# Optimization experiments

Measured on AMD Instinct MI355X. Metric: run time of the kernel, lower is better.

The kernel has to match this reference:

```python
import jax, jax.numpy as jnp
import numpy as np
from math import factorial, sqrt

# Irreps config (all even parity): (mul, l)
IRREPS_IN1 = [(128, 0), (64, 1), (32, 2)]   # dim 480
IRREPS_IN2 = [(1, 0), (1, 1), (1, 2)]       # dim 9
OUT_LS = (0, 1, 2)
Z = 50000


def _su2_cg(j1, j2, j3, m1, m2, m3):
    """Complex SU(2) Clebsch-Gordan coefficient <j1 m1 j2 m2 | j3 m3> (integer l)."""
    if m3 != m1 + m2:
        return 0.0
    pref = sqrt((2 * j3 + 1) * factorial(j3 + j1 - j2) * factorial(j3 - j1 + j2)
                * factorial(j1 + j2 - j3) / factorial(j1 + j2 + j3 + 1))
    pref *= sqrt(factorial(j3 + m3) * factorial(j3 - m3) * factorial(j1 - m1)
                 * factorial(j1 + m1) * factorial(j2 - m2) * factorial(j2 + m2))
    s = 0.0
    for k in range(max(0, j2 - j3 - m1, j1 - j3 + m2),
                   min(j1 + j2 - j3, j1 - m1, j2 + m2) + 1):
        s += (-1) ** k / (factorial(k) * factorial(j1 + j2 - j3 - k)
                          * factorial(j1 - m1 - k) * factorial(j2 + m2 - k)
                          * factorial(j3 - j2 + m1 + k) * factorial(j3 - j1 - m2 + k))
    return pref * s


def _q_real_to_complex(l):
    """e3nn change-of-basis real->complex spherical harmonics."""
    q = np.zeros((2 * l + 1, 2 * l + 1), dtype=np.complex128)
    for m in range(-l, 0):
        q[l + m, l + abs(m)] = 1 / np.sqrt(2)
        q[l + m, l - abs(m)] = -1j / np.sqrt(2)
    q[l, l] = 1.0
    for m in range(1, l + 1):
        q[l + m, l + abs(m)] = (-1) ** m / np.sqrt(2)
        q[l + m, l - abs(m)] = 1j * (-1) ** m / np.sqrt(2)
    return (-1j) ** l * q


def _w3j(l1, l2, l3):
    """Real-basis Wigner 3j tensor, unit Frobenius norm (e3nn convention)."""
    C = np.zeros((2 * l1 + 1, 2 * l2 + 1, 2 * l3 + 1))
    for m1 in range(-l1, l1 + 1):
        for m2 in range(-l2, l2 + 1):
            m3 = m1 + m2
            if -l3 <= m3 <= l3:
                C[l1 + m1, l2 + m2, l3 + m3] = _su2_cg(l1, l2, l3, m1, m2, m3)
    Q1, Q2, Q3 = _q_real_to_complex(l1), _q_real_to_complex(l2), _q_real_to_complex(l3)
    Cr = np.einsum('ij,kl,nm,ikn->jlm', Q1, Q2, np.conj(Q3), C.astype(np.complex128))
    assert np.abs(Cr.imag).max() < 1e-8
    Cr = Cr.real
    return (Cr / np.linalg.norm(Cr)).astype(np.float32)


def _build_instructions():
    off1 = np.cumsum([0] + [m * (2 * l + 1) for m, l in IRREPS_IN1])
    off2 = np.cumsum([0] + [m * (2 * l + 1) for m, l in IRREPS_IN2])
    instrs = []
    for i, (mul1, l1) in enumerate(IRREPS_IN1):
        for j, (mul2, l2) in enumerate(IRREPS_IN2):
            for l3 in range(abs(l1 - l2), l1 + l2 + 1):
                if l3 in OUT_LS or l3 == 0:
                    # path_weight: irrep_normalization='component', path_normalization='element';
                    # each i_out is unique so fan-in = mul2 (uvu num_elements)
                    instrs.append(dict(s1=int(off1[i]), mul1=mul1, l1=l1,
                                       s2=int(off2[j]), mul2=mul2, l2=l2,
                                       l3=l3, pw=sqrt((2 * l3 + 1) / mul2)))
    return instrs


INSTRS = _build_instructions()
DIM1 = sum(m * (2 * l + 1) for m, l in IRREPS_IN1)                 # 480
DIM2 = sum(m * (2 * l + 1) for m, l in IRREPS_IN2)                 # 9
WEIGHT_NUMEL = sum(i['mul1'] * i['mul2'] for i in INSTRS)          # 960
DIM_OUT = sum(i['mul1'] * (2 * i['l3'] + 1) for i in INSTRS)       # 3136
W3J = {(l1, l2, l3): jnp.asarray(_w3j(l1, l2, l3))
       for (l1, l2, l3) in {(i['l1'], i['l2'], i['l3']) for i in INSTRS}}


def setup_inputs() -> dict:
    key = jax.random.key(0)
    k1, k2, k3 = jax.random.split(key, 3)
    x = jax.random.normal(k1, (Z, DIM1), dtype=jnp.float32)
    y = jax.random.normal(k2, (Z, DIM2), dtype=jnp.float32)
    weight = jax.random.normal(k3, (Z, WEIGHT_NUMEL), dtype=jnp.float32)
    return {"x": x, "y": y, "weight": weight}


def reference(x, y, weight):
    z = x.shape[0]
    outs = []
    wo = 0
    for ins in INSTRS:
        mul1, l1, mul2, l2, l3 = ins['mul1'], ins['l1'], ins['mul2'], ins['l2'], ins['l3']
        d1, d2, d3 = 2 * l1 + 1, 2 * l2 + 1, 2 * l3 + 1
        x_s = x[:, ins['s1']:ins['s1'] + mul1 * d1].reshape(z, mul1, d1)
        y_s = y[:, ins['s2']:ins['s2'] + mul2 * d2].reshape(z, mul2, d2)
        w_s = weight[:, wo:wo + mul1 * mul2].reshape(z, mul1, mul2)
        wo += mul1 * mul2
        C = W3J[(l1, l2, l3)]  # [d1, d2, d3]
        # uvu: out[z,u,k] = pw * sum_{v,i,j} w[z,u,v] * C[i,j,k] * x[z,u,i] * y[z,v,j]
        o = ins['pw'] * jnp.einsum('ijk,zui,zvj,zuv->zuk', C, x_s, y_s, w_s)
        outs.append(o.reshape(z, mul1 * d3))
    return jnp.concatenate(outs, axis=-1)  # [Z, 3136]
```

## Files before the change

### kernel.cpp

```cpp
#include <hip/hip_runtime.h>
#include <cmath>
#include <complex>


struct W3JPack {
    float c000[1];
    float c011[9];
    float c022[25];
    float c101[9];
    float c110[9];
    float c111[27];
    float c112[45];
    float c121[45];
    float c122[75];
    float c202[25];
    float c211[45];
    float c212[75];
    float c220[25];
    float c221[75];
    float c222[125];
};

namespace {

using cd = std::complex<double>;

double factd(int n) { double r = 1.0; for (int i = 2; i <= n; ++i) r *= i; return r; }

double su2_cg(int j1, int j2, int j3, int m1, int m2, int m3) {
    if (m3 != m1 + m2) return 0.0;
    double pref = std::sqrt((2.0 * j3 + 1.0) * factd(j3 + j1 - j2) * factd(j3 - j1 + j2)
                            * factd(j1 + j2 - j3) / factd(j1 + j2 + j3 + 1));
    pref *= std::sqrt(factd(j3 + m3) * factd(j3 - m3) * factd(j1 - m1)
                      * factd(j1 + m1) * factd(j2 - m2) * factd(j2 + m2));
    int kmin = 0;
    if (j2 - j3 - m1 > kmin) kmin = j2 - j3 - m1;
    if (j1 - j3 + m2 > kmin) kmin = j1 - j3 + m2;
    int kmax = j1 + j2 - j3;
    if (j1 - m1 < kmax) kmax = j1 - m1;
    if (j2 + m2 < kmax) kmax = j2 + m2;
    double s = 0.0;
    for (int k = kmin; k <= kmax; ++k) {
        double den = factd(k) * factd(j1 + j2 - j3 - k) * factd(j1 - m1 - k)
                   * factd(j2 + m2 - k) * factd(j3 - j2 + m1 + k) * factd(j3 - j1 - m2 + k);
        s += ((k & 1) ? -1.0 : 1.0) / den;
    }
    return pref * s;
}

void qmat(int l, cd q[5][5]) {
    for (int a = 0; a < 5; ++a) for (int b = 0; b < 5; ++b) q[a][b] = cd(0, 0);
    const double is2 = 1.0 / std::sqrt(2.0);
    for (int m = -l; m < 0; ++m) {
        q[l + m][l - m] = cd(is2, 0.0);
        q[l + m][l + m] = cd(0.0, -is2);
    }
    q[l][l] = cd(1.0, 0.0);
    for (int m = 1; m <= l; ++m) {
        double sgn = (m & 1) ? -1.0 : 1.0;
        q[l + m][l + m] = cd(sgn * is2, 0.0);
        q[l + m][l - m] = cd(0.0, sgn * is2);
    }
    cd f(1.0, 0.0);
    const cd mi(0.0, -1.0);
    for (int k = 0; k < l; ++k) f *= mi;
    for (int a = 0; a < 5; ++a) for (int b = 0; b < 5; ++b) q[a][b] *= f;
}

void w3j_real(int l1, int l2, int l3, float* out, double pw) {
    const int d1 = 2 * l1 + 1, d2 = 2 * l2 + 1, d3 = 2 * l3 + 1;
    cd Q1[5][5], Q2[5][5], Q3[5][5];
    qmat(l1, Q1); qmat(l2, Q2); qmat(l3, Q3);
    double tmp[125];
    double norm2 = 0.0;
    for (int a = 0; a < d1; ++a)
        for (int b = 0; b < d2; ++b)
            for (int c = 0; c < d3; ++c) {
                cd acc(0.0, 0.0);
                for (int i = 0; i < d1; ++i) {
                    int m1 = i - l1;
                    for (int k = 0; k < d2; ++k) {
                        int m2 = k - l2;
                        int m3 = m1 + m2;
                        if (m3 < -l3 || m3 > l3) continue;
                        double cg = su2_cg(l1, l2, l3, m1, m2, m3);
                        if (cg == 0.0) continue;
                        acc += Q1[i][a] * Q2[k][b] * std::conj(Q3[m3 + l3][c]) * cg;
                    }
                }
                double v = acc.real();
                tmp[(a * d2 + b) * d3 + c] = v;
                norm2 += v * v;
            }
    const double scale = pw / std::sqrt(norm2);
    for (int idx = 0; idx < d1 * d2 * d3; ++idx) out[idx] = (float)(tmp[idx] * scale);
}

W3JPack build_pack() {
    W3JPack p;
    const double s3 = std::sqrt(3.0), s5 = std::sqrt(5.0);
    w3j_real(0, 0, 0, p.c000, 1.0);
    w3j_real(0, 1, 1, p.c011, s3);
    w3j_real(0, 2, 2, p.c022, s5);
    w3j_real(1, 0, 1, p.c101, s3);
    w3j_real(1, 1, 0, p.c110, 1.0);
    w3j_real(1, 1, 1, p.c111, s3);
    w3j_real(1, 1, 2, p.c112, s5);
    w3j_real(1, 2, 1, p.c121, s3);
    w3j_real(1, 2, 2, p.c122, s5);
    w3j_real(2, 0, 2, p.c202, s5);
    w3j_real(2, 1, 1, p.c211, s3);
    w3j_real(2, 1, 2, p.c212, s5);
    w3j_real(2, 2, 0, p.c220, 1.0);
    w3j_real(2, 2, 1, p.c221, s3);
    w3j_real(2, 2, 2, p.c222, s5);
    return p;
}

const W3JPack g_pack = build_pack();

}


__global__ __launch_bounds__(256) void dtp_kernel(
    const float* __restrict__ x, const float* __restrict__ y,
    const float* __restrict__ w, float* __restrict__ out,
    const W3JPack P, int Z)
{
    const int t = blockIdx.x * 256 + threadIdx.x;
    const int N0 = Z * 128;
    const int N1 = Z * 64;

    if (t < N0) {
        const int z = t >> 7, u = t & 127;
        const float* xz = x + (size_t)z * 480;
        const float* yz = y + (size_t)z * 9;
        const float* wz = w + (size_t)z * 960;
        float* oz = out + (size_t)z * 3136;

        const float xv = xz[u];
        const float y0 = yz[0];
        float y1[3], y2[5];
#pragma unroll
        for (int j = 0; j < 3; ++j) y1[j] = yz[1 + j];
#pragma unroll
        for (int j = 0; j < 5; ++j) y2[j] = yz[4 + j];

        oz[u] = wz[u] * (P.c000[0] * xv * y0);
        {
            const float wx = wz[128 + u] * xv;
#pragma unroll
            for (int k = 0; k < 3; ++k) {
                float s = 0.f;
#pragma unroll
                for (int j = 0; j < 3; ++j) s += P.c011[j * 3 + k] * y1[j];
                oz[128 + 3 * u + k] = wx * s;
            }
        }
        {
            const float wx = wz[256 + u] * xv;
#pragma unroll
            for (int k = 0; k < 5; ++k) {
                float s = 0.f;
#pragma unroll
                for (int j = 0; j < 5; ++j) s += P.c022[j * 5 + k] * y2[j];
                oz[512 + 5 * u + k] = wx * s;
            }
        }
    } else if (t < N0 + N1) {
        const int tt = t - N0;
        const int z = tt >> 6, u = tt & 63;
        const float* xz = x + (size_t)z * 480 + 128 + 3 * u;
        const float* yz = y + (size_t)z * 9;
        const float* wz = w + (size_t)z * 960;
        float* oz = out + (size_t)z * 3136;

        float xv[3];
#pragma unroll
        for (int i = 0; i < 3; ++i) xv[i] = xz[i];
        const float y0 = yz[0];
        float y1[3], y2[5];
#pragma unroll
        for (int j = 0; j < 3; ++j) y1[j] = yz[1 + j];
#pragma unroll
        for (int j = 0; j < 5; ++j) y2[j] = yz[4 + j];

        float xy1[3][3], xy2[3][5];
#pragma unroll
        for (int i = 0; i < 3; ++i) {
#pragma unroll
            for (int j = 0; j < 3; ++j) xy1[i][j] = xv[i] * y1[j];
#pragma unroll
            for (int j = 0; j < 5; ++j) xy2[i][j] = xv[i] * y2[j];
        }

        {
            const float wy = wz[384 + u] * y0;
#pragma unroll
            for (int k = 0; k < 3; ++k) {
                float s = 0.f;
#pragma unroll
                for (int i = 0; i < 3; ++i) s += P.c101[i * 3 + k] * xv[i];
                oz[1152 + 3 * u + k] = wy * s;
            }
        }
        {
            float s = 0.f;
#pragma unroll
            for (int i = 0; i < 3; ++i)
#pragma unroll
                for (int j = 0; j < 3; ++j) s += P.c110[i * 3 + j] * xy1[i][j];
            oz[1344 + u] = wz[448 + u] * s;
        }
        {
            const float wv = wz[512 + u];
#pragma unroll
            for (int k = 0; k < 3; ++k) {
                float s = 0.f;
#pragma unroll
                for (int i = 0; i < 3; ++i)
#pragma unroll
                    for (int j = 0; j < 3; ++j) s += P.c111[(i * 3 + j) * 3 + k] * xy1[i][j];
                oz[1408 + 3 * u + k] = wv * s;
            }
        }
        {
            const float wv = wz[576 + u];
#pragma unroll
            for (int k = 0; k < 5; ++k) {
                float s = 0.f;
#pragma unroll
                for (int i = 0; i < 3; ++i)
#pragma unroll
                    for (int j = 0; j < 3; ++j) s += P.c112[(i * 3 + j) * 5 + k] * xy1[i][j];
                oz[1600 + 5 * u + k] = wv * s;
            }
        }
        {
            const float wv = wz[640 + u];
#pragma unroll
            for (int k = 0; k < 3; ++k) {
                float s = 0.f;
#pragma unroll
                for (int i = 0; i < 3; ++i)
#pragma unroll
                    for (int j = 0; j < 5; ++j) s += P.c121[(i * 5 + j) * 3 + k] * xy2[i][j];
                oz[1920 + 3 * u + k] = wv * s;
            }
        }
        {
            const float wv = wz[704 + u];
#pragma unroll
            for (int k = 0; k < 5; ++k) {
                float s = 0.f;
#pragma unroll
                for (int i = 0; i < 3; ++i)
#pragma unroll
                    for (int j = 0; j < 5; ++j) s += P.c122[(i * 5 + j) * 5 + k] * xy2[i][j];
                oz[2112 + 5 * u + k] = wv * s;
            }
        }
    } else {
        const int tt = t - N0 - N1;
        if (tt >= Z * 32) return;
        const int z = tt >> 5, u = tt & 31;
        const float* xz = x + (size_t)z * 480 + 320 + 5 * u;
        const float* yz = y + (size_t)z * 9;
        const float* wz = w + (size_t)z * 960;
        float* oz = out + (size_t)z * 3136;

        float xv[5];
#pragma unroll
        for (int i = 0; i < 5; ++i) xv[i] = xz[i];
        const float y0 = yz[0];
        float y1[3], y2[5];
#pragma unroll
        for (int j = 0; j < 3; ++j) y1[j] = yz[1 + j];
#pragma unroll
        for (int j = 0; j < 5; ++j) y2[j] = yz[4 + j];

        float xy1[5][3], xy2[5][5];
#pragma unroll
        for (int i = 0; i < 5; ++i) {
#pragma unroll
            for (int j = 0; j < 3; ++j) xy1[i][j] = xv[i] * y1[j];
#pragma unroll
            for (int j = 0; j < 5; ++j) xy2[i][j] = xv[i] * y2[j];
        }

        {
            const float wy = wz[768 + u] * y0;
#pragma unroll
            for (int k = 0; k < 5; ++k) {
                float s = 0.f;
#pragma unroll
                for (int i = 0; i < 5; ++i) s += P.c202[i * 5 + k] * xv[i];
                oz[2432 + 5 * u + k] = wy * s;
            }
        }
        {
            const float wv = wz[800 + u];
#pragma unroll
            for (int k = 0; k < 3; ++k) {
                float s = 0.f;
#pragma unroll
                for (int i = 0; i < 5; ++i)
#pragma unroll
                    for (int j = 0; j < 3; ++j) s += P.c211[(i * 3 + j) * 3 + k] * xy1[i][j];
                oz[2592 + 3 * u + k] = wv * s;
            }
        }
        {
            const float wv = wz[832 + u];
#pragma unroll
            for (int k = 0; k < 5; ++k) {
                float s = 0.f;
#pragma unroll
                for (int i = 0; i < 5; ++i)
#pragma unroll
                    for (int j = 0; j < 3; ++j) s += P.c212[(i * 3 + j) * 5 + k] * xy1[i][j];
                oz[2688 + 5 * u + k] = wv * s;
            }
        }
        {
            float s = 0.f;
#pragma unroll
            for (int i = 0; i < 5; ++i)
#pragma unroll
                for (int j = 0; j < 5; ++j) s += P.c220[i * 5 + j] * xy2[i][j];
            oz[2848 + u] = wz[864 + u] * s;
        }
        {
            const float wv = wz[896 + u];
#pragma unroll
            for (int k = 0; k < 3; ++k) {
                float s = 0.f;
#pragma unroll
                for (int i = 0; i < 5; ++i)
#pragma unroll
                    for (int j = 0; j < 5; ++j) s += P.c221[(i * 5 + j) * 3 + k] * xy2[i][j];
                oz[2880 + 3 * u + k] = wv * s;
            }
        }
        {
            const float wv = wz[928 + u];
#pragma unroll
            for (int k = 0; k < 5; ++k) {
                float s = 0.f;
#pragma unroll
                for (int i = 0; i < 5; ++i)
#pragma unroll
                    for (int j = 0; j < 5; ++j) s += P.c222[(i * 5 + j) * 5 + k] * xy2[i][j];
                oz[2976 + 5 * u + k] = wv * s;
            }
        }
    }
}

extern "C" void kernel_launch(void* const* d_in, const int* in_sizes, int n_in,
                              void* d_out, int out_size, void* d_ws, size_t ws_size,
                              hipStream_t stream)
{
    const float* x = (const float*)d_in[0];
    const float* y = (const float*)d_in[1];
    const float* w = (const float*)d_in[2];
    float* out = (float*)d_out;

    const int Z = in_sizes[0] / 480;
    const int total = Z * 224;
    const int grid = (total + 255) / 256;

    hipLaunchKernelGGL(dtp_kernel, dim3(grid), dim3(256), 0, stream,
                       x, y, w, out, g_pack, Z);
}
```

Baseline: 191.7 us.

## Coalesce strided loads and stores via per-wave LDS transpose buffers

Per-thread strided accesses of 3 or 5 consecutive floats, in both the x loads and the multi-component output stores, are replaced by a per-wavefront shared-memory exchange. Each wave writes its values contiguously into LDS and then issues unit-stride global accesses, so every global instruction touches one contiguous span. This targets uncoalesced memory traffic in a bandwidth-bound kernel. The cost is extra LDS traffic, wave barriers and some bank conflicts, and the code relies on each wave mapping to a single z row, which holds given the 64/128/32 thread layout.

```diff
diff --git a/kernel.cpp b/kernel.cpp
--- a/kernel.cpp
+++ b/kernel.cpp
@@ -119,6 +119,61 @@
 
 const W3JPack g_pack = build_pack();
 
+
+}
+
+template<int K>
+__device__ __forceinline__ void xchg_store(float* __restrict__ base,
+                                           const float (&v)[K],
+                                           float* __restrict__ buf, int ln)
+{
+#pragma unroll
+    for (int k = 0; k < K; ++k) buf[K * ln + k] = v[k];
+    __builtin_amdgcn_wave_barrier();
+#pragma unroll
+    for (int s = 0; s < K; ++s) base[64 * s + ln] = buf[64 * s + ln];
+    __builtin_amdgcn_wave_barrier();
+}
+
+template<int K>
+__device__ __forceinline__ void xchg_load(const float* __restrict__ base,
+                                          float (&v)[K],
+                                          float* __restrict__ buf, int ln)
+{
+#pragma unroll
+    for (int s = 0; s < K; ++s) buf[64 * s + ln] = base[64 * s + ln];
+    __builtin_amdgcn_wave_barrier();
+#pragma unroll
+    for (int k = 0; k < K; ++k) v[k] = buf[K * ln + k];
+    __builtin_amdgcn_wave_barrier();
+}
+
+template<int K>
+__device__ __forceinline__ void half_store(float* __restrict__ base_half,
+                                           const float (&v)[K],
+                                           float* __restrict__ buf, int li, int half)
+{
+    float* b = buf + half * K * 32;
+#pragma unroll
+    for (int k = 0; k < K; ++k) b[K * li + k] = v[k];
+    __builtin_amdgcn_wave_barrier();
+#pragma unroll
+    for (int s = 0; s < K; ++s) base_half[32 * s + li] = b[32 * s + li];
+    __builtin_amdgcn_wave_barrier();
+}
+
+template<int K>
+__device__ __forceinline__ void half_load(const float* __restrict__ base_half,
+                                          float (&v)[K],
+                                          float* __restrict__ buf, int li, int half)
+{
+    float* b = buf + half * K * 32;
+#pragma unroll
+    for (int s = 0; s < K; ++s) b[32 * s + li] = base_half[32 * s + li];
+    __builtin_amdgcn_wave_barrier();
+#pragma unroll
+    for (int k = 0; k < K; ++k) v[k] = b[K * li + k];
+    __builtin_amdgcn_wave_barrier();
 }
 
 
@@ -127,12 +182,17 @@
     const float* __restrict__ w, float* __restrict__ out,
     const W3JPack P, int Z)
 {
+    __shared__ float xch[4][320];
+    const int ln = threadIdx.x & 63;
+    float* buf = xch[threadIdx.x >> 6];
+
     const int t = blockIdx.x * 256 + threadIdx.x;
     const int N0 = Z * 128;
     const int N1 = Z * 64;
 
     if (t < N0) {
         const int z = t >> 7, u = t & 127;
+        const int u0 = u & ~63;
         const float* xz = x + (size_t)z * 480;
         const float* yz = y + (size_t)z * 9;
         const float* wz = w + (size_t)z * 960;
@@ -147,37 +207,42 @@
         for (int j = 0; j < 5; ++j) y2[j] = yz[4 + j];
 
         oz[u] = wz[u] * (P.c000[0] * xv * y0);
+
         {
             const float wx = wz[128 + u] * xv;
+            float o[3];
 #pragma unroll
             for (int k = 0; k < 3; ++k) {
                 float s = 0.f;
 #pragma unroll
                 for (int j = 0; j < 3; ++j) s += P.c011[j * 3 + k] * y1[j];
-                oz[128 + 3 * u + k] = wx * s;
-            }
+                o[k] = wx * s;
+            }
+            xchg_store<3>(oz + 128 + 3 * u0, o, buf, ln);
         }
         {
             const float wx = wz[256 + u] * xv;
+            float o[5];
 #pragma unroll
             for (int k = 0; k < 5; ++k) {
                 float s = 0.f;
 #pragma unroll
                 for (int j = 0; j < 5; ++j) s += P.c022[j * 5 + k] * y2[j];
-                oz[512 + 5 * u + k] = wx * s;
-            }
+                o[k] = wx * s;
+            }
+            xchg_store<5>(oz + 512 + 5 * u0, o, buf, ln);
         }
     } else if (t < N0 + N1) {
         const int tt = t - N0;
-        const int z = tt >> 6, u = tt & 63;
-        const float* xz = x + (size_t)z * 480 + 128 + 3 * u;
+        const int z = tt >> 6;
+        const int u = ln;
         const float* yz = y + (size_t)z * 9;
         const float* wz = w + (size_t)z * 960;
         float* oz = out + (size_t)z * 3136;
 
         float xv[3];
-#pragma unroll
-        for (int i = 0; i < 3; ++i) xv[i] = xz[i];
+        xchg_load<3>(x + (size_t)z * 480 + 128, xv, buf, ln);
+
         const float y0 = yz[0];
         float y1[3], y2[5];
 #pragma unroll
@@ -196,13 +261,15 @@
 
         {
             const float wy = wz[384 + u] * y0;
+            float o[3];
 #pragma unroll
             for (int k = 0; k < 3; ++k) {
                 float s = 0.f;
 #pragma unroll
                 for (int i = 0; i < 3; ++i) s += P.c101[i * 3 + k] * xv[i];
-                oz[1152 + 3 * u + k] = wy * s;
-            }
+                o[k] = wy * s;
+            }
+            xchg_store<3>(oz + 1152, o, buf, ln);
         }
         {
             float s = 0.f;
@@ -214,6 +281,7 @@
         }
         {
             const float wv = wz[512 + u];
+            float o[3];
 #pragma unroll
             for (int k = 0; k < 3; ++k) {
                 float s = 0.f;
@@ -221,11 +289,13 @@
                 for (int i = 0; i < 3; ++i)
 #pragma unroll
                     for (int j = 0; j < 3; ++j) s += P.c111[(i * 3 + j) * 3 + k] * xy1[i][j];
-                oz[1408 + 3 * u + k] = wv * s;
-            }
+                o[k] = wv * s;
+            }
+            xchg_store<3>(oz + 1408, o, buf, ln);
         }
         {
             const float wv = wz[576 + u];
+            float o[5];
 #pragma unroll
             for (int k = 0; k < 5; ++k) {
                 float s = 0.f;
@@ -233,11 +303,13 @@
                 for (int i = 0; i < 3; ++i)
 #pragma unroll
                     for (int j = 0; j < 3; ++j) s += P.c112[(i * 3 + j) * 5 + k] * xy1[i][j];
-                oz[1600 + 5 * u + k] = wv * s;
-            }
+                o[k] = wv * s;
+            }
+            xchg_store<5>(oz + 1600, o, buf, ln);
         }
         {
             const float wv = wz[640 + u];
+            float o[3];
 #pragma unroll
             for (int k = 0; k < 3; ++k) {
                 float s = 0.f;
@@ -245,11 +317,13 @@
                 for (int i = 0; i < 3; ++i)
 #pragma unroll
                     for (int j = 0; j < 5; ++j) s += P.c121[(i * 5 + j) * 3 + k] * xy2[i][j];
-                oz[1920 + 3 * u + k] = wv * s;
-            }
+                o[k] = wv * s;
+            }
+            xchg_store<3>(oz + 1920, o, buf, ln);
         }
         {
             const float wv = wz[704 + u];
+            float o[5];
 #pragma unroll
             for (int k = 0; k < 5; ++k) {
                 float s = 0.f;
@@ -257,21 +331,23 @@
                 for (int i = 0; i < 3; ++i)
 #pragma unroll
                     for (int j = 0; j < 5; ++j) s += P.c122[(i * 5 + j) * 5 + k] * xy2[i][j];
-                oz[2112 + 5 * u + k] = wv * s;
-            }
+                o[k] = wv * s;
+            }
+            xchg_store<5>(oz + 2112, o, buf, ln);
         }
     } else {
         const int tt = t - N0 - N1;
         if (tt >= Z * 32) return;
-        const int z = tt >> 5, u = tt & 31;
-        const float* xz = x + (size_t)z * 480 + 320 + 5 * u;
+        const int z = tt >> 5;
+        const int u = tt & 31;
+        const int li = ln & 31, half = ln >> 5;
         const float* yz = y + (size_t)z * 9;
         const float* wz = w + (size_t)z * 960;
         float* oz = out + (size_t)z * 3136;
 
         float xv[5];
-#pragma unroll
-        for (int i = 0; i < 5; ++i) xv[i] = xz[i];
+        half_load<5>(x + (size_t)z * 480 + 320, xv, buf, li, half);
+
         const float y0 = yz[0];
         float y1[3], y2[5];
 #pragma unroll
@@ -290,16 +366,19 @@
 
         {
             const float wy = wz[768 + u] * y0;
+            float o[5];
 #pragma unroll
             for (int k = 0; k < 5; ++k) {
                 float s = 0.f;
 #pragma unroll
                 for (int i = 0; i < 5; ++i) s += P.c202[i * 5 + k] * xv[i];
-                oz[2432 + 5 * u + k] = wy * s;
-            }
+                o[k] = wy * s;
+            }
+            half_store<5>(oz + 2432, o, buf, li, half);
         }
         {
             const float wv = wz[800 + u];
+            float o[3];
 #pragma unroll
             for (int k = 0; k < 3; ++k) {
                 float s = 0.f;
@@ -307,11 +386,13 @@
                 for (int i = 0; i < 5; ++i)
 #pragma unroll
                     for (int j = 0; j < 3; ++j) s += P.c211[(i * 3 + j) * 3 + k] * xy1[i][j];
-                oz[2592 + 3 * u + k] = wv * s;
-            }
+                o[k] = wv * s;
+            }
+            half_store<3>(oz + 2592, o, buf, li, half);
         }
         {
             const float wv = wz[832 + u];
+            float o[5];
 #pragma unroll
             for (int k = 0; k < 5; ++k) {
                 float s = 0.f;
@@ -319,8 +400,9 @@
                 for (int i = 0; i < 5; ++i)
 #pragma unroll
                     for (int j = 0; j < 3; ++j) s += P.c212[(i * 3 + j) * 5 + k] * xy1[i][j];
-                oz[2688 + 5 * u + k] = wv * s;
-            }
+                o[k] = wv * s;
+            }
+            half_store<5>(oz + 2688, o, buf, li, half);
         }
         {
             float s = 0.f;
@@ -332,6 +414,7 @@
         }
         {
             const float wv = wz[896 + u];
+            float o[3];
 #pragma unroll
             for (int k = 0; k < 3; ++k) {
                 float s = 0.f;
@@ -339,11 +422,13 @@
                 for (int i = 0; i < 5; ++i)
 #pragma unroll
                     for (int j = 0; j < 5; ++j) s += P.c221[(i * 5 + j) * 3 + k] * xy2[i][j];
-                oz[2880 + 3 * u + k] = wv * s;
-            }
+                o[k] = wv * s;
+            }
+            half_store<3>(oz + 2880, o, buf, li, half);
         }
         {
             const float wv = wz[928 + u];
+            float o[5];
 #pragma unroll
             for (int k = 0; k < 5; ++k) {
                 float s = 0.f;
@@ -351,8 +436,9 @@
                 for (int i = 0; i < 5; ++i)
 #pragma unroll
                     for (int j = 0; j < 5; ++j) s += P.c222[(i * 5 + j) * 5 + k] * xy2[i][j];
-                oz[2976 + 5 * u + k] = wv * s;
-            }
+                o[k] = wv * s;
+            }
+            half_store<5>(oz + 2976, o, buf, li, half);
         }
     }
 }
```

Measured after the change: 186.6 us. 2.7% less time.

## Stage outputs in per-wave LDS and write with coalesced float4 stores; interleave block types

Applied to the files above, without the earlier changes.

Each wave now writes its results into a per-wave shared-memory buffer and then stores them to global memory as contiguous float4 vectors, replacing the strided per-lane scalar stores. The x inputs for l=1 and l=2 are loaded the same way, vectorised through LDS. A block-index swizzle interleaves l0, l1 and l2 work within groups of seven blocks so the different per-thread costs are spread across the GPU, and the row index is made wave-uniform with readfirstlane. The change adds about 22 KB of LDS per block, which may lower occupancy. It relies on wave-level barriers and on the wave size being 64.

```diff
diff --git a/kernel.cpp b/kernel.cpp
--- a/kernel.cpp
+++ b/kernel.cpp
@@ -125,20 +125,201 @@
 __global__ __launch_bounds__(256) void dtp_kernel(
     const float* __restrict__ x, const float* __restrict__ y,
     const float* __restrict__ w, float* __restrict__ out,
-    const W3JPack P, int Z)
+    const W3JPack P, int Z, int swz)
 {
-    const int t = blockIdx.x * 256 + threadIdx.x;
+    __shared__ __align__(16) float xch[4][1408];
+    const int tid = threadIdx.x;
+    const int ln = tid & 63;
+    float* buf = xch[tid >> 6];
+    float4* bf4 = (float4*)buf;
+
     const int N0 = Z * 128;
     const int N1 = Z * 64;
 
+    int t;
+    if (swz) {
+        const int bid = blockIdx.x;
+        const int q = bid / 7, r = bid - 7 * q;
+        if (r < 4)       t = (4 * q + r) * 256 + tid;
+        else if (r < 6)  t = N0 + (2 * q + (r - 4)) * 256 + tid;
+        else             t = N0 + N1 + q * 256 + tid;
+    } else {
+        t = blockIdx.x * 256 + tid;
+        if (t >= Z * 224) return;
+    }
+
     if (t < N0) {
         const int z = t >> 7, u = t & 127;
-        const float* xz = x + (size_t)z * 480;
+        const int u0 = u & 64;
+        const int zu = __builtin_amdgcn_readfirstlane(z);
+        const float* xz = x + (size_t)zu * 480;
+        const float* yz = y + (size_t)zu * 9;
+        const float* wz = w + (size_t)zu * 960;
+        float* oz = out + (size_t)zu * 3136;
+
+        const float xv = xz[u];
+        const float y0 = yz[0];
+        float y1[3], y2[5];
+#pragma unroll
+        for (int j = 0; j < 3; ++j) y1[j] = yz[1 + j];
+#pragma unroll
+        for (int j = 0; j < 5; ++j) y2[j] = yz[4 + j];
+
+        buf[ln] = wz[u] * (P.c000[0] * xv * y0);
+        {
+            const float wx = wz[128 + u] * xv;
+#pragma unroll
+            for (int k = 0; k < 3; ++k) {
+                float s = 0.f;
+#pragma unroll
+                for (int j = 0; j < 3; ++j) s += P.c011[j * 3 + k] * y1[j];
+                buf[64 + 3 * ln + k] = wx * s;
+            }
+        }
+        {
+            const float wx = wz[256 + u] * xv;
+#pragma unroll
+            for (int k = 0; k < 5; ++k) {
+                float s = 0.f;
+#pragma unroll
+                for (int j = 0; j < 5; ++j) s += P.c022[j * 5 + k] * y2[j];
+                buf[256 + 5 * ln + k] = wx * s;
+            }
+        }
+        __builtin_amdgcn_wave_barrier();
+        if (ln < 16) *(float4*)(oz + u0 + 4 * ln) = bf4[ln];
+        if (ln < 48) *(float4*)(oz + 128 + 3 * u0 + 4 * ln) = bf4[16 + ln];
+        *(float4*)(oz + 512 + 5 * u0 + 4 * ln) = bf4[64 + ln];
+        if (ln < 16) *(float4*)(oz + 512 + 5 * u0 + 256 + 4 * ln) = bf4[128 + ln];
+        __builtin_amdgcn_wave_barrier();
+    } else if (t < N0 + N1) {
+        const int tt = t - N0;
+        const int z = tt >> 6;
+        const int u = ln;
+        const int zu = __builtin_amdgcn_readfirstlane(z);
+        const float* yz = y + (size_t)zu * 9;
+        const float* wz = w + (size_t)zu * 960;
+        float* oz = out + (size_t)zu * 3136;
+
+        {
+            const float4* xs = (const float4*)(x + (size_t)zu * 480 + 128);
+            if (ln < 48) *(float4*)(buf + 4 * ln) = xs[ln];
+        }
+        __builtin_amdgcn_wave_barrier();
+        float xv[3];
+#pragma unroll
+        for (int i = 0; i < 3; ++i) xv[i] = buf[3 * ln + i];
+        __builtin_amdgcn_wave_barrier();
+
+        const float y0 = yz[0];
+        float y1[3], y2[5];
+#pragma unroll
+        for (int j = 0; j < 3; ++j) y1[j] = yz[1 + j];
+#pragma unroll
+        for (int j = 0; j < 5; ++j) y2[j] = yz[4 + j];
+
+        float xy1[3][3], xy2[3][5];
+#pragma unroll
+        for (int i = 0; i < 3; ++i) {
+#pragma unroll
+            for (int j = 0; j < 3; ++j) xy1[i][j] = xv[i] * y1[j];
+#pragma unroll
+            for (int j = 0; j < 5; ++j) xy2[i][j] = xv[i] * y2[j];
+        }
+
+        {
+            const float wy = wz[384 + u] * y0;
+#pragma unroll
+            for (int k = 0; k < 3; ++k) {
+                float s = 0.f;
+#pragma unroll
+                for (int i = 0; i < 3; ++i) s += P.c101[i * 3 + k] * xv[i];
+                buf[3 * ln + k] = wy * s;
+            }
+        }
+        {
+            float s = 0.f;
+#pragma unroll
+            for (int i = 0; i < 3; ++i)
+#pragma unroll
+                for (int j = 0; j < 3; ++j) s += P.c110[i * 3 + j] * xy1[i][j];
+            buf[192 + ln] = wz[448 + u] * s;
+        }
+        {
+            const float wv = wz[512 + u];
+#pragma unroll
+            for (int k = 0; k < 3; ++k) {
+                float s = 0.f;
+#pragma unroll
+                for (int i = 0; i < 3; ++i)
+#pragma unroll
+                    for (int j = 0; j < 3; ++j) s += P.c111[(i * 3 + j) * 3 + k] * xy1[i][j];
+                buf[256 + 3 * ln + k] = wv * s;
+            }
+        }
+        {
+            const float wv = wz[576 + u];
+#pragma unroll
+            for (int k = 0; k < 5; ++k) {
+                float s = 0.f;
+#pragma unroll
+                for (int i = 0; i < 3; ++i)
+#pragma unroll
+                    for (int j = 0; j < 3; ++j) s += P.c112[(i * 3 + j) * 5 + k] * xy1[i][j];
+                buf[448 + 5 * ln + k] = wv * s;
+            }
+        }
+        {
+            const float wv = wz[640 + u];
+#pragma unroll
+            for (int k = 0; k < 3; ++k) {
+                float s = 0.f;
+#pragma unroll
+                for (int i = 0; i < 3; ++i)
+#pragma unroll
+                    for (int j = 0; j < 5; ++j) s += P.c121[(i * 5 + j) * 3 + k] * xy2[i][j];
+                buf[768 + 3 * ln + k] = wv * s;
+            }
+        }
+        {
+            const float wv = wz[704 + u];
+#pragma unroll
+            for (int k = 0; k < 5; ++k) {
+                float s = 0.f;
+#pragma unroll
+                for (int i = 0; i < 3; ++i)
+#pragma unroll
+                    for (int j = 0; j < 5; ++j) s += P.c122[(i * 5 + j) * 5 + k] * xy2[i][j];
+                buf[960 + 5 * ln + k] = wv * s;
+            }
+        }
+        __builtin_amdgcn_wave_barrier();
+        float* ob = oz + 1152;
+#pragma unroll
+        for (int it = 0; it < 5; ++it)
+            *(float4*)(ob + 4 * (it * 64 + ln)) = bf4[it * 64 + ln];
+        __builtin_amdgcn_wave_barrier();
+    } else {
+        const int tt = t - N0 - N1;
+        const int li = ln & 31, half = ln >> 5;
+        const int z0 = __builtin_amdgcn_readfirstlane(tt >> 5);
+        const int z = z0 + half;
+        const int u = li;
         const float* yz = y + (size_t)z * 9;
         const float* wz = w + (size_t)z * 960;
         float* oz = out + (size_t)z * 3136;
 
-        const float xv = xz[u];
+        {
+            const float4* xs = (const float4*)(x + (size_t)z * 480 + 320);
+            *(float4*)(buf + 160 * half + 4 * li) = xs[li];
+            if (li < 8) *(float4*)(buf + 160 * half + 128 + 4 * li) = xs[32 + li];
+        }
+        __builtin_amdgcn_wave_barrier();
+        float xv[5];
+#pragma unroll
+        for (int i = 0; i < 5; ++i) xv[i] = buf[160 * half + 5 * li + i];
+        __builtin_amdgcn_wave_barrier();
+
         const float y0 = yz[0];
         float y1[3], y2[5];
 #pragma unroll
@@ -146,214 +327,89 @@
 #pragma unroll
         for (int j = 0; j < 5; ++j) y2[j] = yz[4 + j];
 
-        oz[u] = wz[u] * (P.c000[0] * xv * y0);
-        {
-            const float wx = wz[128 + u] * xv;
-#pragma unroll
-            for (int k = 0; k < 3; ++k) {
-                float s = 0.f;
-#pragma unroll
-                for (int j = 0; j < 3; ++j) s += P.c011[j * 3 + k] * y1[j];
-                oz[128 + 3 * u + k] = wx * s;
-            }
-        }
-        {
-            const float wx = wz[256 + u] * xv;
-#pragma unroll
-            for (int k = 0; k < 5; ++k) {
-                float s = 0.f;
-#pragma unroll
-                for (int j = 0; j < 5; ++j) s += P.c022[j * 5 + k] * y2[j];
-                oz[512 + 5 * u + k] = wx * s;
-            }
-        }
-    } else if (t < N0 + N1) {
-        const int tt = t - N0;
-        const int z = tt >> 6, u = tt & 63;
-        const float* xz = x + (size_t)z * 480 + 128 + 3 * u;
-        const float* yz = y + (size_t)z * 9;
-        const float* wz = w + (size_t)z * 960;
-        float* oz = out + (size_t)z * 3136;
-
-        float xv[3];
-#pragma unroll
-        for (int i = 0; i < 3; ++i) xv[i] = xz[i];
-        const float y0 = yz[0];
-        float y1[3], y2[5];
-#pragma unroll
-        for (int j = 0; j < 3; ++j) y1[j] = yz[1 + j];
-#pragma unroll
-        for (int j = 0; j < 5; ++j) y2[j] = yz[4 + j];
-
-        float xy1[3][3], xy2[3][5];
-#pragma unroll
-        for (int i = 0; i < 3; ++i) {
+        float xy1[5][3], xy2[5][5];
+#pragma unroll
+        for (int i = 0; i < 5; ++i) {
 #pragma unroll
             for (int j = 0; j < 3; ++j) xy1[i][j] = xv[i] * y1[j];
 #pragma unroll
             for (int j = 0; j < 5; ++j) xy2[i][j] = xv[i] * y2[j];
         }
 
-        {
-            const float wy = wz[384 + u] * y0;
-#pragma unroll
-            for (int k = 0; k < 3; ++k) {
-                float s = 0.f;
-#pragma unroll
-                for (int i = 0; i < 3; ++i) s += P.c101[i * 3 + k] * xv[i];
-                oz[1152 + 3 * u + k] = wy * s;
+        float* hb = buf + 704 * half;
+        {
+            const float wy = wz[768 + u] * y0;
+#pragma unroll
+            for (int k = 0; k < 5; ++k) {
+                float s = 0.f;
+#pragma unroll
+                for (int i = 0; i < 5; ++i) s += P.c202[i * 5 + k] * xv[i];
+                hb[5 * li + k] = wy * s;
+            }
+        }
+        {
+            const float wv = wz[800 + u];
+#pragma unroll
+            for (int k = 0; k < 3; ++k) {
+                float s = 0.f;
+#pragma unroll
+                for (int i = 0; i < 5; ++i)
+#pragma unroll
+                    for (int j = 0; j < 3; ++j) s += P.c211[(i * 3 + j) * 3 + k] * xy1[i][j];
+                hb[160 + 3 * li + k] = wv * s;
+            }
+        }
+        {
+            const float wv = wz[832 + u];
+#pragma unroll
+            for (int k = 0; k < 5; ++k) {
+                float s = 0.f;
+#pragma unroll
+                for (int i = 0; i < 5; ++i)
+#pragma unroll
+                    for (int j = 0; j < 3; ++j) s += P.c212[(i * 3 + j) * 5 + k] * xy1[i][j];
+                hb[256 + 5 * li + k] = wv * s;
             }
         }
         {
             float s = 0.f;
 #pragma unroll
-            for (int i = 0; i < 3; ++i)
-#pragma unroll
-                for (int j = 0; j < 3; ++j) s += P.c110[i * 3 + j] * xy1[i][j];
-            oz[1344 + u] = wz[448 + u] * s;
-        }
-        {
-            const float wv = wz[512 + u];
-#pragma unroll
-            for (int k = 0; k < 3; ++k) {
-                float s = 0.f;
-#pragma unroll
-                for (int i = 0; i < 3; ++i)
-#pragma unroll
-                    for (int j = 0; j < 3; ++j) s += P.c111[(i * 3 + j) * 3 + k] * xy1[i][j];
-                oz[1408 + 3 * u + k] = wv * s;
-            }
-        }
-        {
-            const float wv = wz[576 + u];
-#pragma unroll
-            for (int k = 0; k < 5; ++k) {
-                float s = 0.f;
-#pragma unroll
-                for (int i = 0; i < 3; ++i)
-#pragma unroll
-                    for (int j = 0; j < 3; ++j) s += P.c112[(i * 3 + j) * 5 + k] * xy1[i][j];
-                oz[1600 + 5 * u + k] = wv * s;
-            }
-        }
-        {
-            const float wv = wz[640 + u];
-#pragma unroll
-            for (int k = 0; k < 3; ++k) {
-                float s = 0.f;
-#pragma unroll
-                for (int i = 0; i < 3; ++i)
-#pragma unroll
-                    for (int j = 0; j < 5; ++j) s += P.c121[(i * 5 + j) * 3 + k] * xy2[i][j];
-                oz[1920 + 3 * u + k] = wv * s;
-            }
-        }
-        {
-            const float wv = wz[704 + u];
-#pragma unroll
-            for (int k = 0; k < 5; ++k) {
-                float s = 0.f;
-#pragma unroll
-                for (int i = 0; i < 3; ++i)
-#pragma unroll
-                    for (int j = 0; j < 5; ++j) s += P.c122[(i * 5 + j) * 5 + k] * xy2[i][j];
-                oz[2112 + 5 * u + k] = wv * s;
-            }
-        }
-    } else {
-        const int tt = t - N0 - N1;
-        if (tt >= Z * 32) return;
-        const int z = tt >> 5, u = tt & 31;
-        const float* xz = x + (size_t)z * 480 + 320 + 5 * u;
-        const float* yz = y + (size_t)z * 9;
-        const float* wz = w + (size_t)z * 960;
-        float* oz = out + (size_t)z * 3136;
-
-        float xv[5];
-#pragma unroll
-        for (int i = 0; i < 5; ++i) xv[i] = xz[i];
-        const float y0 = yz[0];
-        float y1[3], y2[5];
-#pragma unroll
-        for (int j = 0; j < 3; ++j) y1[j] = yz[1 + j];
-#pragma unroll
-        for (int j = 0; j < 5; ++j) y2[j] = yz[4 + j];
-
-        float xy1[5][3], xy2[5][5];
-#pragma unroll
-        for (int i = 0; i < 5; ++i) {
-#pragma unroll
-            for (int j = 0; j < 3; ++j) xy1[i][j] = xv[i] * y1[j];
-#pragma unroll
-            for (int j = 0; j < 5; ++j) xy2[i][j] = xv[i] * y2[j];
-        }
-
-        {
-            const float wy = wz[768 + u] * y0;
-#pragma unroll
-            for (int k = 0; k < 5; ++k) {
-                float s = 0.f;
-#pragma unroll
-                for (int i = 0; i < 5; ++i) s += P.c202[i * 5 + k] * xv[i];
-                oz[2432 + 5 * u + k] = wy * s;
-            }
-        }
-        {
-            const float wv = wz[800 + u];
+            for (int i = 0; i < 5; ++i)
+#pragma unroll
+                for (int j = 0; j < 5; ++j) s += P.c220[i * 5 + j] * xy2[i][j];
+            hb[416 + li] = wz[864 + u] * s;
+        }
+        {
+            const float wv = wz[896 + u];
 #pragma unroll
             for (int k = 0; k < 3; ++k) {
                 float s = 0.f;
 #pragma unroll
                 for (int i = 0; i < 5; ++i)
 #pragma unroll
-                    for (int j = 0; j < 3; ++j) s += P.c211[(i * 3 + j) * 3 + k] * xy1[i][j];
-                oz[2592 + 3 * u + k] = wv * s;
-            }
-        }
-        {
-            const float wv = wz[832 + u];
+                    for (int j = 0; j < 5; ++j) s += P.c221[(i * 5 + j) * 3 + k] * xy2[i][j];
+                hb[448 + 3 * li + k] = wv * s;
+            }
+        }
+        {
+            const float wv = wz[928 + u];
 #pragma unroll
             for (int k = 0; k < 5; ++k) {
                 float s = 0.f;
 #pragma unroll
                 for (int i = 0; i < 5; ++i)
 #pragma unroll
-                    for (int j = 0; j < 3; ++j) s += P.c212[(i * 3 + j) * 5 + k] * xy1[i][j];
-                oz[2688 + 5 * u + k] = wv * s;
-            }
-        }
-        {
-            float s = 0.f;
-#pragma unroll
-            for (int i = 0; i < 5; ++i)
-#pragma unroll
-                for (int j = 0; j < 5; ++j) s += P.c220[i * 5 + j] * xy2[i][j];
-            oz[2848 + u] = wz[864 + u] * s;
-        }
-        {
-            const float wv = wz[896 + u];
-#pragma unroll
-            for (int k = 0; k < 3; ++k) {
-                float s = 0.f;
-#pragma unroll
-                for (int i = 0; i < 5; ++i)
-#pragma unroll
-                    for (int j = 0; j < 5; ++j) s += P.c221[(i * 5 + j) * 3 + k] * xy2[i][j];
-                oz[2880 + 3 * u + k] = wv * s;
-            }
-        }
-        {
-            const float wv = wz[928 + u];
-#pragma unroll
-            for (int k = 0; k < 5; ++k) {
-                float s = 0.f;
-#pragma unroll
-                for (int i = 0; i < 5; ++i)
-#pragma unroll
                     for (int j = 0; j < 5; ++j) s += P.c222[(i * 5 + j) * 5 + k] * xy2[i][j];
-                oz[2976 + 5 * u + k] = wv * s;
-            }
-        }
+                hb[544 + 5 * li + k] = wv * s;
+            }
+        }
+        __builtin_amdgcn_wave_barrier();
+        float* ob = oz + 2432;
+#pragma unroll
+        for (int it = 0; it < 5; ++it)
+            *(float4*)(ob + 4 * (it * 32 + li)) = *(float4*)(hb + 4 * (it * 32 + li));
+        if (li < 16) *(float4*)(ob + 4 * (160 + li)) = *(float4*)(hb + 4 * (160 + li));
+        __builtin_amdgcn_wave_barrier();
     }
 }
 
@@ -369,7 +425,8 @@
     const int Z = in_sizes[0] / 480;
     const int total = Z * 224;
     const int grid = (total + 255) / 256;
+    const int swz = (Z % 8 == 0) ? 1 : 0;
 
     hipLaunchKernelGGL(dtp_kernel, dim3(grid), dim3(256), 0, stream,
-                       x, y, w, out, g_pack, Z);
-}
+                       x, y, w, out, g_pack, Z, swz);
+}
```

New measurement: 166.9 us. -12.9%, faster.
